# Performance work log

Hardware: AMD Instinct MI355X
Metric: run time of the kernel (lower is better)

Reference implementation:

```python
import jax, jax.numpy as jnp
import numpy as np

E = 8          # number of tasks/experts (grown via new_task in the original)
B = 4096       # batch
CH, HT, WD = 3, 32, 32
D = CH * HT * WD   # 3072 flattened image dim
H = 1024       # hidden_dim
L = 512        # latent_dim
C = 100        # classes
TEMP = 2.0     # self.temperature


def setup_inputs() -> dict:
    key = jax.random.key(0)
    ks = jax.random.split(key, 32)
    def w(k, shape, fan_in):
        return jax.random.normal(k, shape, jnp.float32) * (1.0 / np.sqrt(fan_in))
    z = lambda shape: jnp.zeros(shape, jnp.float32)
    return {
        "x": jax.random.normal(ks[0], (B, CH, HT, WD), jnp.float32),
        # Gate autoencoder (per-expert stacked): encoder D->H->H->L, decoder L->H->H->D
        "enc_w0": w(ks[1], (E, D, H), D), "enc_b0": z((E, H)),
        "enc_w1": w(ks[2], (E, H, H), H), "enc_b1": z((E, H)),
        "enc_w2": w(ks[3], (E, H, L), H), "enc_b2": z((E, L)),
        "dec_w0": w(ks[4], (E, L, H), L), "dec_b0": z((E, H)),
        "dec_w1": w(ks[5], (E, H, H), H), "dec_b1": z((E, H)),
        "dec_w2": w(ks[6], (E, H, D), H), "dec_b2": z((E, D)),
        # Expert MLP (per-expert stacked): L->H->H->C
        "exp_w0": w(ks[7], (E, L, H), L), "exp_b0": z((E, H)),
        "exp_w1": w(ks[8], (E, H, H), H), "exp_b1": z((E, H)),
        "exp_w2": w(ks[9], (E, H, C), H), "exp_b2": z((E, C)),
    }


def reference(x, enc_w0, enc_b0, enc_w1, enc_b1, enc_w2, enc_b2,
              dec_w0, dec_b0, dec_w1, dec_b1, dec_w2, dec_b2,
              exp_w0, exp_b0, exp_w1, exp_b1, exp_w2, exp_b2):
    relu = jax.nn.relu
    b = x.shape[0]
    xf = x.reshape(b, -1)                                            # [B, D]
    # --- all gates in one batched pass (replaces python loop over gates) ---
    h = relu(jnp.einsum('bd,edh->ebh', xf, enc_w0) + enc_b0[:, None, :])
    h = relu(jnp.einsum('ebh,ehk->ebk', h, enc_w1) + enc_b1[:, None, :])
    lat = jnp.einsum('ebh,ehl->ebl', h, enc_w2) + enc_b2[:, None, :]  # [E, B, L]
    g = relu(jnp.einsum('ebl,elh->ebh', lat, dec_w0) + dec_b0[:, None, :])
    g = relu(jnp.einsum('ebh,ehk->ebk', g, dec_w1) + dec_b1[:, None, :])
    recon_flat = jnp.einsum('ebh,ehd->ebd', g, dec_w2) + dec_b2[:, None, :]  # [E, B, D]
    # L1 reconstruction error, mean over (C,H,W) == mean over flattened D
    err = jnp.mean(jnp.abs(recon_flat - xf[None]), axis=-1)          # [E, B]
    relevance_scores = jax.nn.softmax(-err / TEMP, axis=0)           # softmax over experts
    indices = jnp.argmin(err, axis=0)                                # [B]
    min_err = jnp.min(err, axis=0)                                   # [B]
    mask = jnp.arange(err.shape[0])[:, None] == indices[None, :]     # [E, B] bool
    # --- all experts densely, then select per-sample winner (same math as
    # the original masked gather/MLP/scatter: each row gets its argmin expert) ---
    e = relu(jnp.einsum('ebl,elh->ebh', lat, exp_w0) + exp_b0[:, None, :])
    e = relu(jnp.einsum('ebh,ehk->ebk', e, exp_w1) + exp_b1[:, None, :])
    exp_out = jnp.einsum('ebh,ehc->ebc', e, exp_w2) + exp_b2[:, None, :]  # [E, B, C]
    logits = jnp.take_along_axis(exp_out, indices[None, :, None], axis=0)[0]  # [B, C]
    reconstructions = recon_flat.reshape((err.shape[0],) + x.shape)  # [E, B, C, H, W]
    return (logits, reconstructions, indices, min_err, relevance_scores, mask)
```

## Files before the change

### kernel.cpp

```cpp
#include <hip/hip_runtime.h>
#include <hip/hip_fp16.h>

#define E_ 8
#define B_ 4096
#define D_ 3072
#define H_ 1024
#define L_ 512
#define C_ 100

#define RECON_OFF  409600ull
#define IDX_OFF    101072896ull
#define MINERR_OFF 101076992ull
#define REL_OFF    101081088ull
#define MASK_OFF   101113856ull

typedef _Float16 half8 __attribute__((ext_vector_type(8)));
typedef float floatx4 __attribute__((ext_vector_type(4)));

#define AS1 __attribute__((address_space(1)))
#define AS3 __attribute__((address_space(3)))

__device__ __forceinline__ void gl16(const void* g, void* l) {
  __builtin_amdgcn_global_load_lds((const AS1 unsigned int*)g, (AS3 unsigned int*)l, 16, 0, 0);
}

enum { OM_HILO = 0, OM_HI = 1, OM_F32 = 2, OM_RECON = 3 };

template <int OM, bool RELU, bool SPLIT>
__launch_bounds__(256, SPLIT ? 3 : 4)
__global__ void gemm_k(const _Float16* __restrict__ Ah, const _Float16* __restrict__ Al,
                       const _Float16* __restrict__ Bh, const _Float16* __restrict__ Bl,
                       const float* __restrict__ bias, int biasN,
                       _Float16* __restrict__ Oh, _Float16* __restrict__ Ol,
                       float* __restrict__ Of, const float* __restrict__ Xf,
                       float* __restrict__ errOut,
                       int N, int K, int Npad, int Nstore, long aStrideE)
{
  const int M = B_;
  const int mBlocks = M >> 7;
  const int bx = blockIdx.x;
  const int mb = bx % mBlocks;
  const int nb = bx / mBlocks;
  const int e = blockIdx.y;
  const int m0 = mb << 7, n0 = nb << 7;
  const int tid = threadIdx.x;
  const int wave = tid >> 6, lane = tid & 63;
  const int wy = wave >> 1, wx = wave & 1;
  const int q = lane >> 4, t = lane & 15;

  __shared__ __align__(16) _Float16 sAh[128 * 32];
  __shared__ __align__(16) _Float16 sBh[128 * 32];
  __shared__ __align__(16) _Float16 sAl[SPLIT ? 128 * 32 : 8];
  __shared__ __align__(16) _Float16 sBl[SPLIT ? 128 * 32 : 8];
  __shared__ float ebuf[OM == OM_RECON ? 256 : 1];

  const int swzc = ((lane & 3) ^ ((lane >> 3) & 3)) * 8;
  const size_t aoff = (size_t)(m0 + wave * 32 + (lane >> 2)) * K + swzc;
  const size_t boff = (size_t)(n0 + wave * 32 + (lane >> 2)) * K + swzc;
  const _Float16* pAh = Ah + (size_t)e * aStrideE + aoff;
  const _Float16* pBh = Bh + (size_t)e * Npad * K + boff;
  const _Float16* pAl = SPLIT ? (Al + (size_t)e * aStrideE + aoff) : (const _Float16*)nullptr;
  const _Float16* pBl = SPLIT ? (Bl + (size_t)e * Npad * K + boff) : (const _Float16*)nullptr;
  _Float16* dAh = &sAh[(wave * 32) * 32];
  _Float16* dBh = &sBh[(wave * 32) * 32];
  _Float16* dAl = &sAl[SPLIT ? (wave * 32) * 32 : 0];
  _Float16* dBl = &sBl[SPLIT ? (wave * 32) * 32 : 0];

  const int rcol = (q ^ ((t >> 1) & 3)) * 8;

  floatx4 acc[4][4] = {};

  for (int kt = 0; kt < K; kt += 32) {
    __syncthreads();
    gl16(pAh, dAh);
    gl16(pAh + (size_t)16 * K, dAh + 16 * 32);
    gl16(pBh, dBh);
    gl16(pBh + (size_t)16 * K, dBh + 16 * 32);
    if (SPLIT) {
      gl16(pAl, dAl);
      gl16(pAl + (size_t)16 * K, dAl + 16 * 32);
      gl16(pBl, dBl);
      gl16(pBl + (size_t)16 * K, dBl + 16 * 32);
    }
    pAh += 32; pBh += 32;
    if (SPLIT) { pAl += 32; pBl += 32; }
    __syncthreads();

    half8 a_h[4], b_h[4], a_l[4], b_l[4];
#pragma unroll
    for (int i = 0; i < 4; ++i) {
      a_h[i] = *(const half8*)&sAh[(wy * 64 + i * 16 + t) * 32 + rcol];
      b_h[i] = *(const half8*)&sBh[(wx * 64 + i * 16 + t) * 32 + rcol];
      if (SPLIT) {
        a_l[i] = *(const half8*)&sAl[(wy * 64 + i * 16 + t) * 32 + rcol];
        b_l[i] = *(const half8*)&sBl[(wx * 64 + i * 16 + t) * 32 + rcol];
      }
    }
#pragma unroll
    for (int i = 0; i < 4; ++i)
#pragma unroll
      for (int j = 0; j < 4; ++j) {
        acc[i][j] = __builtin_amdgcn_mfma_f32_16x16x32_f16(a_h[i], b_h[j], acc[i][j], 0, 0, 0);
        if (SPLIT) {
          acc[i][j] = __builtin_amdgcn_mfma_f32_16x16x32_f16(a_h[i], b_l[j], acc[i][j], 0, 0, 0);
          acc[i][j] = __builtin_amdgcn_mfma_f32_16x16x32_f16(a_l[i], b_h[j], acc[i][j], 0, 0, 0);
        }
      }
  }

  float esum[4][4];
#pragma unroll
  for (int i = 0; i < 4; ++i)
#pragma unroll
    for (int r = 0; r < 4; ++r) esum[i][r] = 0.0f;

#pragma unroll
  for (int j = 0; j < 4; ++j) {
    const int gcol = n0 + wx * 64 + j * 16 + t;
    float bj = 0.0f;
    if (OM == OM_F32) { if (gcol < biasN) bj = bias[e * biasN + gcol]; }
    else bj = bias[e * biasN + gcol];
#pragma unroll
    for (int i = 0; i < 4; ++i)
#pragma unroll
      for (int r = 0; r < 4; ++r) {
        float v = acc[i][j][r] + bj;
        if (RELU) v = fmaxf(v, 0.0f);
        const int grow = m0 + wy * 64 + i * 16 + q * 4 + r;
        if (OM == OM_HILO) {
          const size_t o = (size_t)e * M * N + (size_t)grow * N + gcol;
          _Float16 h = (_Float16)v;
          Oh[o] = h;
          Ol[o] = (_Float16)(v - (float)h);
        } else if (OM == OM_HI) {
          Oh[(size_t)e * M * N + (size_t)grow * N + gcol] = (_Float16)v;
        } else if (OM == OM_F32) {
          if (gcol < Nstore)
            Of[(size_t)e * M * Nstore + (size_t)grow * Nstore + gcol] = v;
        } else {
          const size_t o = (size_t)e * M * N + (size_t)grow * N + gcol;
          Of[o] = v;
          esum[i][r] += fabsf(v - Xf[(size_t)grow * N + gcol]);
        }
      }
  }

  if (OM == OM_RECON) {
#pragma unroll
    for (int i = 0; i < 4; ++i)
#pragma unroll
      for (int r = 0; r < 4; ++r) {
        float s = esum[i][r];
        s += __shfl_xor(s, 1, 16);
        s += __shfl_xor(s, 2, 16);
        s += __shfl_xor(s, 4, 16);
        s += __shfl_xor(s, 8, 16);
        if (t == 0) ebuf[(wy * 64 + i * 16 + q * 4 + r) * 2 + wx] = s;
      }
    __syncthreads();
    if (tid < 128)
      atomicAdd(&errOut[(size_t)e * M + m0 + tid], ebuf[tid * 2] + ebuf[tid * 2 + 1]);
  }
}

__global__ void xsplit_k(const float* __restrict__ x, _Float16* __restrict__ xh,
                         _Float16* __restrict__ xl, int n)
{
  int i = blockIdx.x * 256 + threadIdx.x;
  if (i < n) {
    float v = x[i];
    _Float16 h = (_Float16)v;
    xh[i] = h;
    xl[i] = (_Float16)(v - (float)h);
  }
}

__global__ void wprep_k(const float* __restrict__ W, _Float16* __restrict__ Th,
                        _Float16* __restrict__ Tl, int K, int N, int Npad)
{
  __shared__ float tile[32][33];
  const int e = blockIdx.z;
  const int k0 = blockIdx.x * 32, n0 = blockIdx.y * 32;
  const int tx = threadIdx.x, ty = threadIdx.y;
  const float* We = W + (size_t)e * K * N;
#pragma unroll
  for (int s = 0; s < 4; ++s) {
    int k = k0 + ty + s * 8, n = n0 + tx;
    tile[ty + s * 8][tx] = (n < N) ? We[(size_t)k * N + n] : 0.0f;
  }
  __syncthreads();
#pragma unroll
  for (int s = 0; s < 4; ++s) {
    int n = n0 + ty + s * 8, k = k0 + tx;
    float v = tile[tx][ty + s * 8];
    size_t o = ((size_t)e * Npad + n) * K + k;
    _Float16 h = (_Float16)v;
    Th[o] = h;
    if (Tl) Tl[o] = (_Float16)(v - (float)h);
  }
}

__global__ void finalize_k(const float* __restrict__ err, float* __restrict__ out,
                           int* __restrict__ idxbuf)
{
  int b = blockIdx.x * 256 + threadIdx.x;
  if (b >= B_) return;
  float ev[E_];
  float mn = 3.4e38f;
  int am = 0;
#pragma unroll
  for (int e = 0; e < E_; ++e) {
    float v = err[(size_t)e * B_ + b] * (1.0f / 3072.0f);
    ev[e] = v;
    if (v < mn) { mn = v; am = e; }
  }
  float den = 0.0f, w[E_];
#pragma unroll
  for (int e = 0; e < E_; ++e) { w[e] = expf((mn - ev[e]) * 0.5f); den += w[e]; }
  float inv = 1.0f / den;
  out[IDX_OFF + b] = (float)am;
  out[MINERR_OFF + b] = mn;
#pragma unroll
  for (int e = 0; e < E_; ++e) {
    out[REL_OFF + (size_t)e * B_ + b] = w[e] * inv;
    out[MASK_OFF + (size_t)e * B_ + b] = (e == am) ? 1.0f : 0.0f;
  }
  idxbuf[b] = am;
}

__global__ void gather_k(const float* __restrict__ expout, const int* __restrict__ idx,
                         float* __restrict__ out)
{
  int b = blockIdx.x;
  int c = threadIdx.x;
  if (c < C_) out[(size_t)b * C_ + c] = expout[((size_t)idx[b] * B_ + b) * C_ + c];
}

extern "C" void kernel_launch(void* const* d_in, const int* in_sizes, int n_in,
                              void* d_out, int out_size, void* d_ws, size_t ws_size,
                              hipStream_t stream)
{
  const float* x      = (const float*)d_in[0];
  const float* enc_w0 = (const float*)d_in[1];
  const float* enc_b0 = (const float*)d_in[2];
  const float* enc_w1 = (const float*)d_in[3];
  const float* enc_b1 = (const float*)d_in[4];
  const float* enc_w2 = (const float*)d_in[5];
  const float* enc_b2 = (const float*)d_in[6];
  const float* dec_w0 = (const float*)d_in[7];
  const float* dec_b0 = (const float*)d_in[8];
  const float* dec_w1 = (const float*)d_in[9];
  const float* dec_b1 = (const float*)d_in[10];
  const float* dec_w2 = (const float*)d_in[11];
  const float* dec_b2 = (const float*)d_in[12];
  const float* exp_w0 = (const float*)d_in[13];
  const float* exp_b0 = (const float*)d_in[14];
  const float* exp_w1 = (const float*)d_in[15];
  const float* exp_b1 = (const float*)d_in[16];
  const float* exp_w2 = (const float*)d_in[17];
  const float* exp_b2 = (const float*)d_in[18];

  char* ws = (char*)d_ws;
  _Float16* xh     = (_Float16*)(ws + 0);
  _Float16* xl     = (_Float16*)(ws + 25165824);
  _Float16* WTh    = (_Float16*)(ws + 50331648);
  _Float16* WTl    = (_Float16*)(ws + 100663296);
  _Float16* lath   = (_Float16*)(ws + 150994944);
  _Float16* latl   = (_Float16*)(ws + 184549376);
  _Float16* g2h    = (_Float16*)(ws + 218103808);
  _Float16* g2l    = (_Float16*)(ws + 285212672);
  float*    expout = (float*)   (ws + 352321536);
  float*    errb   = (float*)   (ws + 365428736);
  int*      idxb   = (int*)     (ws + 365559808);

  float* out = (float*)d_out;
  float* recon = out + RECON_OFF;
  _Float16* bufAh = (_Float16*)recon;
  _Float16* bufAl = bufAh + (size_t)E_ * B_ * H_;
  _Float16* bufBh = bufAl + (size_t)E_ * B_ * H_;
  _Float16* bufBl = bufBh + (size_t)E_ * B_ * H_;

  hipMemsetAsync(errb, 0, (size_t)E_ * B_ * 4, stream);
  xsplit_k<<<(B_ * D_ + 255) / 256, 256, 0, stream>>>(x, xh, xl, B_ * D_);

  dim3 wb(32, 8);

  wprep_k<<<dim3(96, 32, E_), wb, 0, stream>>>(enc_w0, WTh, WTl, 3072, 1024, 1024);
  gemm_k<OM_HILO, true, true><<<dim3(32 * 8, E_), 256, 0, stream>>>(
      xh, xl, WTh, WTl, enc_b0, 1024, bufAh, bufAl, nullptr, nullptr, nullptr,
      1024, 3072, 1024, 1024, 0L);
  wprep_k<<<dim3(32, 32, E_), wb, 0, stream>>>(enc_w1, WTh, WTl, 1024, 1024, 1024);
  gemm_k<OM_HILO, true, true><<<dim3(32 * 8, E_), 256, 0, stream>>>(
      bufAh, bufAl, WTh, WTl, enc_b1, 1024, bufBh, bufBl, nullptr, nullptr, nullptr,
      1024, 1024, 1024, 1024, (long)B_ * H_);
  wprep_k<<<dim3(32, 16, E_), wb, 0, stream>>>(enc_w2, WTh, WTl, 1024, 512, 512);
  gemm_k<OM_HILO, false, true><<<dim3(32 * 4, E_), 256, 0, stream>>>(
      bufBh, bufBl, WTh, WTl, enc_b2, 512, lath, latl, nullptr, nullptr, nullptr,
      512, 1024, 512, 512, (long)B_ * H_);
  wprep_k<<<dim3(16, 32, E_), wb, 0, stream>>>(exp_w0, WTh, nullptr, 512, 1024, 1024);
  gemm_k<OM_HI, true, false><<<dim3(32 * 8, E_), 256, 0, stream>>>(
      lath, nullptr, WTh, nullptr, exp_b0, 1024, bufAh, nullptr, nullptr, nullptr, nullptr,
      1024, 512, 1024, 1024, (long)B_ * L_);
  wprep_k<<<dim3(32, 32, E_), wb, 0, stream>>>(exp_w1, WTh, nullptr, 1024, 1024, 1024);
  gemm_k<OM_HI, true, false><<<dim3(32 * 8, E_), 256, 0, stream>>>(
      bufAh, nullptr, WTh, nullptr, exp_b1, 1024, bufBh, nullptr, nullptr, nullptr, nullptr,
      1024, 1024, 1024, 1024, (long)B_ * H_);
  wprep_k<<<dim3(32, 4, E_), wb, 0, stream>>>(exp_w2, WTh, nullptr, 1024, 100, 128);
  gemm_k<OM_F32, false, false><<<dim3(32 * 1, E_), 256, 0, stream>>>(
      bufBh, nullptr, WTh, nullptr, exp_b2, 100, nullptr, nullptr, expout, nullptr, nullptr,
      128, 1024, 128, 100, (long)B_ * H_);
  wprep_k<<<dim3(16, 32, E_), wb, 0, stream>>>(dec_w0, WTh, WTl, 512, 1024, 1024);
  gemm_k<OM_HILO, true, true><<<dim3(32 * 8, E_), 256, 0, stream>>>(
      lath, latl, WTh, WTl, dec_b0, 1024, bufAh, bufAl, nullptr, nullptr, nullptr,
      1024, 512, 1024, 1024, (long)B_ * L_);
  wprep_k<<<dim3(32, 32, E_), wb, 0, stream>>>(dec_w1, WTh, WTl, 1024, 1024, 1024);
  gemm_k<OM_HILO, true, true><<<dim3(32 * 8, E_), 256, 0, stream>>>(
      bufAh, bufAl, WTh, WTl, dec_b1, 1024, g2h, g2l, nullptr, nullptr, nullptr,
      1024, 1024, 1024, 1024, (long)B_ * H_);
  wprep_k<<<dim3(32, 96, E_), wb, 0, stream>>>(dec_w2, WTh, WTl, 1024, 3072, 3072);
  gemm_k<OM_RECON, false, true><<<dim3(32 * 24, E_), 256, 0, stream>>>(
      g2h, g2l, WTh, WTl, dec_b2, 3072, nullptr, nullptr, recon, x, errb,
      3072, 1024, 3072, 3072, (long)B_ * H_);

  finalize_k<<<(B_ + 255) / 256, 256, 0, stream>>>(errb, out, idxb);
  gather_k<<<B_, 128, 0, stream>>>(expout, idxb, out);
}
```

Measured before the change: 2.806 ms.

## Add 256x256-tile split-fp16 GEMM kernel with staged LDS pipeline for gate layers

Adds a new 512-thread GEMM kernel that computes 256x256 output tiles per block using hi/lo fp16 split MFMA, and uses it for all six gate autoencoder GEMMs. The kernel double-buffers LDS via direct global-to-LDS loads, interleaves the staging of the next tile with MFMA sub-phases, and raises wave priority around the MFMA bursts. The larger tile is meant to raise arithmetic intensity and cut global and LDS traffic per FLOP. In exchange it uses about 128KB of LDS and many accumulator registers per block, and it launches far fewer blocks per GEMM, so occupancy and wave balance across CUs may suffer.

Measured after the change: 3.605 ms. 28.5% more time.

```diff
diff --git a/kernel.cpp b/kernel.cpp
--- a/kernel.cpp
+++ b/kernel.cpp
@@ -25,6 +25,170 @@
 }
 
 enum { OM_HILO = 0, OM_HI = 1, OM_F32 = 2, OM_RECON = 3 };
+
+
+#define LDAH(CUR, m) (*(const half8*)&sA_h[CUR][aRd + (m) * 512])
+#define LDAL(CUR, m) (*(const half8*)&sA_l[CUR][aRd + (m) * 512])
+#define LDBH(CUR, n) (*(const half8*)&sB_h[CUR][bRd + (n) * 512])
+#define LDBL(CUR, n) (*(const half8*)&sB_l[CUR][bRd + (n) * 512])
+
+#define STAGE2(PTR, ARR, NXT, ktn)                                        \
+    gl16(PTR + (ktn), &ARR[NXT][wave << 9]);                              \
+    gl16(PTR + (ktn) + rstep, &ARR[NXT][(wave << 9) + 4096]);
+
+#define TILE(CUR, NXT, sg, ktn)                                           \
+  do {                                                                    \
+    half8 ah[8], bh[4], bl[4], alq[4];                                    \
+                                          \
+    _Pragma("unroll") for (int m = 0; m < 4; ++m) ah[m] = LDAH(CUR, m);   \
+    _Pragma("unroll") for (int n = 0; n < 4; ++n) bh[n] = LDBH(CUR, n);   \
+    if (sg) { STAGE2(gAh, sA_h, NXT, ktn) }                               \
+    __builtin_amdgcn_s_barrier();                                         \
+    asm volatile("s_waitcnt lgkmcnt(0)" ::: "memory");                    \
+    __builtin_amdgcn_s_setprio(1);                                        \
+    _Pragma("unroll") for (int m = 0; m < 4; ++m)                         \
+      _Pragma("unroll") for (int n = 0; n < 4; ++n)                       \
+        acc[m][n] = __builtin_amdgcn_mfma_f32_16x16x32_f16(ah[m], bh[n], acc[m][n], 0, 0, 0); \
+    __builtin_amdgcn_s_setprio(0);                                        \
+    __builtin_amdgcn_s_barrier();                                         \
+                                          \
+    _Pragma("unroll") for (int m = 4; m < 8; ++m) ah[m] = LDAH(CUR, m);   \
+    if (sg) { STAGE2(gBh, sB_h, NXT, ktn) }                               \
+    __builtin_amdgcn_s_barrier();                                         \
+    asm volatile("s_waitcnt lgkmcnt(0)" ::: "memory");                    \
+    __builtin_amdgcn_s_setprio(1);                                        \
+    _Pragma("unroll") for (int m = 4; m < 8; ++m)                         \
+      _Pragma("unroll") for (int n = 0; n < 4; ++n)                       \
+        acc[m][n] = __builtin_amdgcn_mfma_f32_16x16x32_f16(ah[m], bh[n], acc[m][n], 0, 0, 0); \
+    __builtin_amdgcn_s_setprio(0);                                        \
+    if (sg) { asm volatile("s_waitcnt vmcnt(4)" ::: "memory"); }          \
+    else    { asm volatile("s_waitcnt vmcnt(0)" ::: "memory"); }          \
+    __builtin_amdgcn_s_barrier();                                         \
+                                   \
+    _Pragma("unroll") for (int n = 0; n < 4; ++n) bl[n] = LDBL(CUR, n);   \
+    if (sg) { STAGE2(gAl, sA_l, NXT, ktn) }                               \
+    __builtin_amdgcn_s_barrier();                                         \
+    asm volatile("s_waitcnt lgkmcnt(0)" ::: "memory");                    \
+    __builtin_amdgcn_s_setprio(1);                                        \
+    _Pragma("unroll") for (int m = 0; m < 8; ++m)                         \
+      _Pragma("unroll") for (int n = 0; n < 4; ++n)                       \
+        acc[m][n] = __builtin_amdgcn_mfma_f32_16x16x32_f16(ah[m], bl[n], acc[m][n], 0, 0, 0); \
+    __builtin_amdgcn_s_setprio(0);                                        \
+    __builtin_amdgcn_s_barrier();                                         \
+             \
+    _Pragma("unroll") for (int m = 0; m < 4; ++m) alq[m] = LDAL(CUR, m);  \
+    if (sg) { STAGE2(gBl, sB_l, NXT, ktn) }                               \
+    __builtin_amdgcn_s_barrier();                                         \
+    asm volatile("s_waitcnt lgkmcnt(0)" ::: "memory");                    \
+    __builtin_amdgcn_s_setprio(1);                                        \
+    _Pragma("unroll") for (int m = 0; m < 4; ++m)                         \
+      _Pragma("unroll") for (int n = 0; n < 4; ++n)                       \
+        acc[m][n] = __builtin_amdgcn_mfma_f32_16x16x32_f16(alq[m], bh[n], acc[m][n], 0, 0, 0); \
+    _Pragma("unroll") for (int m = 0; m < 4; ++m) alq[m] = LDAL(CUR, m + 4); \
+    _Pragma("unroll") for (int m = 0; m < 4; ++m)                         \
+      _Pragma("unroll") for (int n = 0; n < 4; ++n)                       \
+        acc[m + 4][n] = __builtin_amdgcn_mfma_f32_16x16x32_f16(alq[m], bh[n], acc[m + 4][n], 0, 0, 0); \
+    __builtin_amdgcn_s_setprio(0);                                        \
+    if (sg) { asm volatile("s_waitcnt vmcnt(4)" ::: "memory"); }          \
+    __builtin_amdgcn_s_barrier();                                         \
+  } while (0)
+
+template <int OM, bool RELU>
+__launch_bounds__(512, 2)
+__global__ void gemm256_k(const _Float16* __restrict__ Ah, const _Float16* __restrict__ Al,
+                          const _Float16* __restrict__ Bh, const _Float16* __restrict__ Bl,
+                          const float* __restrict__ bias,
+                          _Float16* __restrict__ Oh, _Float16* __restrict__ Ol,
+                          float* __restrict__ Of, const float* __restrict__ Xf,
+                          float* __restrict__ errOut,
+                          int N, int K, long aStrideE)
+{
+  const int bx = blockIdx.x;
+  const int mb = bx & 15, nb = bx >> 4;
+  const int e = blockIdx.y;
+  const int m0 = mb << 8, n0 = nb << 8;
+  const int tid = threadIdx.x;
+  const int wave = tid >> 6, lane = tid & 63;
+  const int wy = wave >> 2, wx = wave & 3;
+  const int q = lane >> 4, t = lane & 15;
+
+  __shared__ __align__(16) _Float16 sA_h[2][8192];
+  __shared__ __align__(16) _Float16 sB_h[2][8192];
+  __shared__ __align__(16) _Float16 sA_l[2][8192];
+  __shared__ __align__(16) _Float16 sB_l[2][8192];
+  __shared__ float ebuf[OM == OM_RECON ? 1024 : 4];
+
+  const int sc8 = (((lane & 3) ^ ((lane >> 3) & 3)) << 3);
+  const size_t aoff = (size_t)(m0 + (wave << 4) + (lane >> 2)) * K + sc8;
+  const size_t boff = (size_t)(n0 + (wave << 4) + (lane >> 2)) * K + sc8;
+  const _Float16* gAh = Ah + (size_t)e * aStrideE + aoff;
+  const _Float16* gAl = Al + (size_t)e * aStrideE + aoff;
+  const _Float16* gBh = Bh + (size_t)e * (size_t)N * K + boff;
+  const _Float16* gBl = Bl + (size_t)e * (size_t)N * K + boff;
+  const size_t rstep = (size_t)128 * K;
+
+  const int rsw = ((q ^ ((t >> 1) & 3)) << 3);
+  const int aRd = ((wy << 7) + t) * 32 + rsw;
+  const int bRd = ((wx << 6) + t) * 32 + rsw;
+
+  floatx4 acc[8][4] = {};
+
+  STAGE2(gAh, sA_h, 0, 0)
+  STAGE2(gBh, sB_h, 0, 0)
+  STAGE2(gAl, sA_l, 0, 0)
+  STAGE2(gBl, sB_l, 0, 0)
+  asm volatile("s_waitcnt vmcnt(4)" ::: "memory");
+  __builtin_amdgcn_s_barrier();
+
+  for (int kt = 0; kt < K; kt += 64) {
+    const bool sgB = (kt + 64) < K;
+    TILE(0, 1, true, kt + 32);
+    TILE(1, 0, sgB, kt + 64);
+  }
+
+  float esum[8][4] = {};
+
+#pragma unroll
+  for (int n = 0; n < 4; ++n) {
+    const int gcol = n0 + (wx << 6) + n * 16 + t;
+    const float bj = bias[e * N + gcol];
+#pragma unroll
+    for (int m = 0; m < 8; ++m)
+#pragma unroll
+      for (int r = 0; r < 4; ++r) {
+        float v = acc[m][n][r] + bj;
+        if (RELU) v = fmaxf(v, 0.0f);
+        const int grow = m0 + (wy << 7) + m * 16 + q * 4 + r;
+        const size_t o = (size_t)e * B_ * N + (size_t)grow * N + gcol;
+        if (OM == OM_HILO) {
+          _Float16 h = (_Float16)v;
+          Oh[o] = h;
+          Ol[o] = (_Float16)(v - (float)h);
+        } else {
+          Of[o] = v;
+          esum[m][r] += fabsf(v - Xf[(size_t)grow * N + gcol]);
+        }
+      }
+  }
+
+  if (OM == OM_RECON) {
+#pragma unroll
+    for (int m = 0; m < 8; ++m)
+#pragma unroll
+      for (int r = 0; r < 4; ++r) {
+        float s = esum[m][r];
+        s += __shfl_xor(s, 1, 16);
+        s += __shfl_xor(s, 2, 16);
+        s += __shfl_xor(s, 4, 16);
+        s += __shfl_xor(s, 8, 16);
+        if (t == 0) ebuf[((wy << 7) + m * 16 + q * 4 + r) * 4 + wx] = s;
+      }
+    __syncthreads();
+    if (tid < 256)
+      atomicAdd(&errOut[(size_t)e * B_ + m0 + tid],
+                ebuf[tid * 4] + ebuf[tid * 4 + 1] + ebuf[tid * 4 + 2] + ebuf[tid * 4 + 3]);
+  }
+}
 
 template <int OM, bool RELU, bool SPLIT>
 __launch_bounds__(256, SPLIT ? 3 : 4)
@@ -286,17 +450,17 @@
   dim3 wb(32, 8);
 
   wprep_k<<<dim3(96, 32, E_), wb, 0, stream>>>(enc_w0, WTh, WTl, 3072, 1024, 1024);
-  gemm_k<OM_HILO, true, true><<<dim3(32 * 8, E_), 256, 0, stream>>>(
-      xh, xl, WTh, WTl, enc_b0, 1024, bufAh, bufAl, nullptr, nullptr, nullptr,
-      1024, 3072, 1024, 1024, 0L);
+  gemm256_k<OM_HILO, true><<<dim3(16 * 4, E_), 512, 0, stream>>>(
+      xh, xl, WTh, WTl, enc_b0, bufAh, bufAl, nullptr, nullptr, nullptr,
+      1024, 3072, 0L);
   wprep_k<<<dim3(32, 32, E_), wb, 0, stream>>>(enc_w1, WTh, WTl, 1024, 1024, 1024);
-  gemm_k<OM_HILO, true, true><<<dim3(32 * 8, E_), 256, 0, stream>>>(
-      bufAh, bufAl, WTh, WTl, enc_b1, 1024, bufBh, bufBl, nullptr, nullptr, nullptr,
-      1024, 1024, 1024, 1024, (long)B_ * H_);
+  gemm256_k<OM_HILO, true><<<dim3(16 * 4, E_), 512, 0, stream>>>(
+      bufAh, bufAl, WTh, WTl, enc_b1, bufBh, bufBl, nullptr, nullptr, nullptr,
+      1024, 1024, (long)B_ * H_);
   wprep_k<<<dim3(32, 16, E_), wb, 0, stream>>>(enc_w2, WTh, WTl, 1024, 512, 512);
-  gemm_k<OM_HILO, false, true><<<dim3(32 * 4, E_), 256, 0, stream>>>(
-      bufBh, bufBl, WTh, WTl, enc_b2, 512, lath, latl, nullptr, nullptr, nullptr,
-      512, 1024, 512, 512, (long)B_ * H_);
+  gemm256_k<OM_HILO, false><<<dim3(16 * 2, E_), 512, 0, stream>>>(
+      bufBh, bufBl, WTh, WTl, enc_b2, lath, latl, nullptr, nullptr, nullptr,
+      512, 1024, (long)B_ * H_);
   wprep_k<<<dim3(16, 32, E_), wb, 0, stream>>>(exp_w0, WTh, nullptr, 512, 1024, 1024);
   gemm_k<OM_HI, true, false><<<dim3(32 * 8, E_), 256, 0, stream>>>(
       lath, nullptr, WTh, nullptr, exp_b0, 1024, bufAh, nullptr, nullptr, nullptr, nullptr,
@@ -310,17 +474,17 @@
       bufBh, nullptr, WTh, nullptr, exp_b2, 100, nullptr, nullptr, expout, nullptr, nullptr,
       128, 1024, 128, 100, (long)B_ * H_);
   wprep_k<<<dim3(16, 32, E_), wb, 0, stream>>>(dec_w0, WTh, WTl, 512, 1024, 1024);
-  gemm_k<OM_HILO, true, true><<<dim3(32 * 8, E_), 256, 0, stream>>>(
-      lath, latl, WTh, WTl, dec_b0, 1024, bufAh, bufAl, nullptr, nullptr, nullptr,
-      1024, 512, 1024, 1024, (long)B_ * L_);
+  gemm256_k<OM_HILO, true><<<dim3(16 * 4, E_), 512, 0, stream>>>(
+      lath, latl, WTh, WTl, dec_b0, bufAh, bufAl, nullptr, nullptr, nullptr,
+      1024, 512, (long)B_ * L_);
   wprep_k<<<dim3(32, 32, E_), wb, 0, stream>>>(dec_w1, WTh, WTl, 1024, 1024, 1024);
-  gemm_k<OM_HILO, true, true><<<dim3(32 * 8, E_), 256, 0, stream>>>(
-      bufAh, bufAl, WTh, WTl, dec_b1, 1024, g2h, g2l, nullptr, nullptr, nullptr,
-      1024, 1024, 1024, 1024, (long)B_ * H_);
+  gemm256_k<OM_HILO, true><<<dim3(16 * 4, E_), 512, 0, stream>>>(
+      bufAh, bufAl, WTh, WTl, dec_b1, g2h, g2l, nullptr, nullptr, nullptr,
+      1024, 1024, (long)B_ * H_);
   wprep_k<<<dim3(32, 96, E_), wb, 0, stream>>>(dec_w2, WTh, WTl, 1024, 3072, 3072);
-  gemm_k<OM_RECON, false, true><<<dim3(32 * 24, E_), 256, 0, stream>>>(
-      g2h, g2l, WTh, WTl, dec_b2, 3072, nullptr, nullptr, recon, x, errb,
-      3072, 1024, 3072, 3072, (long)B_ * H_);
+  gemm256_k<OM_RECON, false><<<dim3(16 * 12, E_), 512, 0, stream>>>(
+      g2h, g2l, WTh, WTl, dec_b2, nullptr, nullptr, recon, x, errb,
+      3072, 1024, (long)B_ * H_);
 
   finalize_k<<<(B_ + 255) / 256, 256, 0, stream>>>(errb, out, idxb);
   gather_k<<<B_, 128, 0, stream>>>(expout, idxb, out);
```
